# Optimization experiments

Hardware: AMD Instinct MI355X
Metric: run time of the kernel (lower is better)

Reference implementation:

```python
import jax, jax.numpy as jnp
import numpy as np

MAX_ITER = 15
EPSILON = 1e-4


def setup_inputs() -> dict:
    key = jax.random.key(0)
    # [B, N, M] non-negative matching scores
    s = jax.random.uniform(key, (32, 1024, 1024), dtype=jnp.float32)
    return {"s": s}


def reference(s) -> jnp.ndarray:
    # Sinkhorn.forward with defaults -> forward_pai:
    # alternate column-sum (dim=1) and row-sum (dim=2) normalization.
    def body(i, s):
        # i even -> sum over dim 1, i odd -> sum over dim 2
        sum1 = jnp.sum(s, axis=1, keepdims=True)  # [B,1,M]
        sum2 = jnp.sum(s, axis=2, keepdims=True)  # [B,N,1]
        sum_s = jnp.where(i % 2 == 1, sum2, sum1 * jnp.ones_like(sum2))
        # broadcasting: sum1 broadcasts along N, sum2 along M; to keep a
        # single where we expand both to full shape lazily via division.
        denom = jnp.where(i % 2 == 1,
                          jnp.broadcast_to(sum2, s.shape),
                          jnp.broadcast_to(sum1, s.shape))
        return s / (denom + EPSILON)

    # fixed small iteration count; unrolled Python loop keeps each step's
    # reduction axis static (cheaper than the lax.fori where-select above).
    for i in range(MAX_ITER):
        axis = 2 if i % 2 == 1 else 1
        sum_s = jnp.sum(s, axis=axis, keepdims=True)
        s = s / (sum_s + EPSILON)
    return s
```

## Files before the change

kernel.cpp:

```cpp
#include <hip/hip_runtime.h>


#define EPSF 1e-4f
constexpr int B_      = 32;
constexpr int N_      = 1024;
constexpr int M_      = 1024;
constexpr int ICHUNK  = 32;
constexpr int NCHUNKS = N_ / ICHUNK;
constexpr int THREADS = 256;

typedef _Float16 half4v __attribute__((ext_vector_type(4)));
typedef _Float16 half8v __attribute__((ext_vector_type(8)));
typedef float    f32x4  __attribute__((ext_vector_type(4)));

__global__ __launch_bounds__(THREADS)
void colsum_conv_kernel(const float* __restrict__ s0,
                        _Float16* __restrict__ sh,
                        float* __restrict__ upart)
{
    const int bid = blockIdx.x, t = threadIdx.x;
    const int b = bid % B_, chunk = bid / B_;
    const int i0 = chunk * ICHUNK;

    const size_t base4 = ((size_t)b * N_ + i0) * (M_ / 4);
    const f32x4* s4 = reinterpret_cast<const f32x4*>(s0) + base4;
    half4v*      o4 = reinterpret_cast<half4v*>(sh) + base4;

    f32x4 acc = {0.f, 0.f, 0.f, 0.f};
    #pragma unroll 4
    for (int i = 0; i < ICHUNK; ++i) {
        const f32x4 sv = s4[(size_t)i * (M_ / 4) + t];
        acc += sv;
        half4v h;
        h[0] = (_Float16)sv.x; h[1] = (_Float16)sv.y;
        h[2] = (_Float16)sv.z; h[3] = (_Float16)sv.w;
        o4[(size_t)i * (M_ / 4) + t] = h;
    }
    reinterpret_cast<f32x4*>(upart + ((size_t)b * NCHUNKS + chunk) * M_)[t] = acc;
}

__global__ __launch_bounds__(THREADS)
void colsum_f16_kernel(const _Float16* __restrict__ sh,
                       const float* __restrict__ rprev,
                       const float* __restrict__ vacc,
                       float* __restrict__ rout,
                       float* __restrict__ upart,
                       int mode)
{
    __shared__ float rS[ICHUNK];
    const int bid = blockIdx.x, t = threadIdx.x;
    const int b = bid % B_, chunk = bid / B_;
    const int i0 = chunk * ICHUNK;

    if (t < ICHUNK) {
        const int gi = b * N_ + i0 + t;
        const float v  = vacc[gi];
        const float rp = (mode == 1) ? 1.0f : rprev[gi];
        const float r  = rp / (rp * v + EPSF);
        rout[gi] = r;
        rS[t] = r;
    }
    __syncthreads();

    const half4v* srow = reinterpret_cast<const half4v*>(sh)
                       + ((size_t)b * N_ + i0) * (M_ / 4);
    f32x4 acc = {0.f, 0.f, 0.f, 0.f};
    #pragma unroll 8
    for (int i = 0; i < ICHUNK; ++i) {
        const float  r  = rS[i];
        const half4v s4 = srow[(size_t)i * (M_ / 4) + t];
        acc.x += r * (float)s4[0]; acc.y += r * (float)s4[1];
        acc.z += r * (float)s4[2]; acc.w += r * (float)s4[3];
    }
    reinterpret_cast<f32x4*>(upart + ((size_t)b * NCHUNKS + chunk) * M_)[t] = acc;
}

__global__ __launch_bounds__(THREADS)
void rowsum_f16_kernel(const _Float16* __restrict__ sh,
                       const float* __restrict__ cprev,
                       const float* __restrict__ upart,
                       float* __restrict__ cout,
                       float* __restrict__ vacc,
                       int mode)
{
    __shared__ float cS[M_];
    const int bid = blockIdx.x, t = threadIdx.x;
    const int b = bid % B_, chunk = bid / B_;
    const int i0 = chunk * ICHUNK;

    {
        f32x4 u4 = {0.f, 0.f, 0.f, 0.f};
        const f32x4* up = reinterpret_cast<const f32x4*>(upart + (size_t)b * NCHUNKS * M_);
        #pragma unroll 8
        for (int ch = 0; ch < NCHUNKS; ++ch)
            u4 += up[ch * (M_ / 4) + t];

        f32x4 cp4 = {1.f, 1.f, 1.f, 1.f};
        if (mode != 1)
            cp4 = reinterpret_cast<const f32x4*>(cprev + b * M_)[t];
        f32x4 c4;
        c4.x = cp4.x / (cp4.x * u4.x + EPSF);
        c4.y = cp4.y / (cp4.y * u4.y + EPSF);
        c4.z = cp4.z / (cp4.z * u4.z + EPSF);
        c4.w = cp4.w / (cp4.w * u4.w + EPSF);
        reinterpret_cast<f32x4*>(cS)[t] = c4;
        if (chunk == 0)
            reinterpret_cast<f32x4*>(cout + b * M_)[t] = c4;
    }
    __syncthreads();

    const int wave = t >> 6, lane = t & 63;
    constexpr int RPW = ICHUNK / 4;

    const f32x4* cS4 = reinterpret_cast<const f32x4*>(cS);
    f32x4 creg[2][2];
    #pragma unroll
    for (int q = 0; q < 2; ++q) {
        creg[q][0] = cS4[2 * (q * 64 + lane)];
        creg[q][1] = cS4[2 * (q * 64 + lane) + 1];
    }

    const half8v* sbase =
        reinterpret_cast<const half8v*>(sh) + (size_t)b * N_ * (M_ / 8);
    #pragma unroll 2
    for (int rw = 0; rw < RPW; ++rw) {
        const int i = i0 + wave * RPW + rw;
        const half8v* row = sbase + (size_t)i * (M_ / 8);
        float sum = 0.f;
        #pragma unroll
        for (int q = 0; q < 2; ++q) {
            const half8v s8 = row[q * 64 + lane];
            sum += (float)s8[0] * creg[q][0].x + (float)s8[1] * creg[q][0].y
                 + (float)s8[2] * creg[q][0].z + (float)s8[3] * creg[q][0].w
                 + (float)s8[4] * creg[q][1].x + (float)s8[5] * creg[q][1].y
                 + (float)s8[6] * creg[q][1].z + (float)s8[7] * creg[q][1].w;
        }
        #pragma unroll
        for (int off = 32; off > 0; off >>= 1)
            sum += __shfl_down(sum, off, 64);
        if (lane == 0)
            vacc[b * N_ + i] = sum;
    }
}

__global__ __launch_bounds__(THREADS)
void colsum_kernel(const float* __restrict__ s0,
                   const float* __restrict__ rprev,
                   const float* __restrict__ vacc,
                   float* __restrict__ rout,
                   float* __restrict__ upart,
                   int mode)
{
    __shared__ float rS[ICHUNK];
    const int bid = blockIdx.x, t = threadIdx.x;
    const int b = bid % B_, chunk = bid / B_;
    const int i0 = chunk * ICHUNK;

    if (t < ICHUNK) {
        const int gi = b * N_ + i0 + t;
        float r;
        if (mode == 0) r = 1.0f;
        else {
            const float v  = vacc[gi];
            const float rp = (mode == 1) ? 1.0f : rprev[gi];
            r = rp / (rp * v + EPSF);
            rout[gi] = r;
        }
        rS[t] = r;
    }
    __syncthreads();

    const f32x4* srow =
        reinterpret_cast<const f32x4*>(s0) + ((size_t)b * N_ + i0) * (M_ / 4);
    f32x4 acc = {0.f, 0.f, 0.f, 0.f};
    #pragma unroll 8
    for (int i = 0; i < ICHUNK; ++i) {
        const float r  = rS[i];
        const f32x4 sv = srow[(size_t)i * (M_ / 4) + t];
        acc.x += r * sv.x; acc.y += r * sv.y;
        acc.z += r * sv.z; acc.w += r * sv.w;
    }
    reinterpret_cast<f32x4*>(upart + ((size_t)b * NCHUNKS + chunk) * M_)[t] = acc;
}

__global__ __launch_bounds__(THREADS)
void rowsum_kernel(const float* __restrict__ s0,
                   const float* __restrict__ cprev,
                   const float* __restrict__ upart,
                   float* __restrict__ cout,
                   float* __restrict__ vacc,
                   int mode)
{
    __shared__ float cS[M_];
    const int bid = blockIdx.x, t = threadIdx.x;
    const int b = bid % B_, chunk = bid / B_;
    const int i0 = chunk * ICHUNK;

    {
        f32x4 u4 = {0.f, 0.f, 0.f, 0.f};
        const f32x4* up = reinterpret_cast<const f32x4*>(upart + (size_t)b * NCHUNKS * M_);
        #pragma unroll 8
        for (int ch = 0; ch < NCHUNKS; ++ch)
            u4 += up[ch * (M_ / 4) + t];

        f32x4 cp4 = {1.f, 1.f, 1.f, 1.f};
        if (mode != 1)
            cp4 = reinterpret_cast<const f32x4*>(cprev + b * M_)[t];
        f32x4 c4;
        c4.x = cp4.x / (cp4.x * u4.x + EPSF);
        c4.y = cp4.y / (cp4.y * u4.y + EPSF);
        c4.z = cp4.z / (cp4.z * u4.z + EPSF);
        c4.w = cp4.w / (cp4.w * u4.w + EPSF);
        reinterpret_cast<f32x4*>(cS)[t] = c4;
        if (chunk == 0)
            reinterpret_cast<f32x4*>(cout + b * M_)[t] = c4;
    }
    __syncthreads();

    const int wave = t >> 6, lane = t & 63;
    constexpr int RPW = ICHUNK / 4;
    const f32x4* cS4 = reinterpret_cast<const f32x4*>(cS);
    f32x4 creg[4];
    #pragma unroll
    for (int q = 0; q < 4; ++q)
        creg[q] = cS4[q * 64 + lane];

    const f32x4* sbase =
        reinterpret_cast<const f32x4*>(s0) + (size_t)b * N_ * (M_ / 4);
    for (int rw = 0; rw < RPW; ++rw) {
        const int i = i0 + wave * RPW + rw;
        const f32x4* row = sbase + (size_t)i * (M_ / 4);
        float sum = 0.f;
        #pragma unroll
        for (int q = 0; q < 4; ++q) {
            const f32x4 sv = row[q * 64 + lane];
            sum += sv.x * creg[q].x + sv.y * creg[q].y +
                   sv.z * creg[q].z + sv.w * creg[q].w;
        }
        #pragma unroll
        for (int off = 32; off > 0; off >>= 1)
            sum += __shfl_down(sum, off, 64);
        if (lane == 0)
            vacc[b * N_ + i] = sum;
    }
}

__global__ __launch_bounds__(THREADS)
void final_kernel(const float* __restrict__ s0,
                  const float* __restrict__ cprev,
                  const float* __restrict__ upart,
                  const float* __restrict__ rbuf,
                  float* __restrict__ out)
{
    __shared__ float rS[ICHUNK];
    const int bid = blockIdx.x, t = threadIdx.x;
    const int b = bid % B_, chunk = bid / B_;
    const int i0 = chunk * ICHUNK;

    f32x4 u4 = {0.f, 0.f, 0.f, 0.f};
    const f32x4* up = reinterpret_cast<const f32x4*>(upart + (size_t)b * NCHUNKS * M_);
    #pragma unroll 8
    for (int ch = 0; ch < NCHUNKS; ++ch)
        u4 += up[ch * (M_ / 4) + t];

    const f32x4 cp4 = reinterpret_cast<const f32x4*>(cprev + b * M_)[t];
    f32x4 c4;
    c4.x = cp4.x / (cp4.x * u4.x + EPSF);
    c4.y = cp4.y / (cp4.y * u4.y + EPSF);
    c4.z = cp4.z / (cp4.z * u4.z + EPSF);
    c4.w = cp4.w / (cp4.w * u4.w + EPSF);

    if (t < ICHUNK) rS[t] = rbuf[b * N_ + i0 + t];
    __syncthreads();

    const size_t base4 = ((size_t)b * N_ + i0) * (M_ / 4);
    const f32x4* sp = reinterpret_cast<const f32x4*>(s0) + base4;
    f32x4*       op = reinterpret_cast<f32x4*>(out) + base4;
    #pragma unroll 4
    for (int i = 0; i < ICHUNK; ++i) {
        const float r  = rS[i];
        const f32x4 sv = sp[(size_t)i * (M_ / 4) + t];
        f32x4 o;
        o.x = r * sv.x * c4.x;
        o.y = r * sv.y * c4.y;
        o.z = r * sv.z * c4.z;
        o.w = r * sv.w * c4.w;
        __builtin_nontemporal_store(o, op + (size_t)i * (M_ / 4) + t);
    }
}

extern "C" void kernel_launch(void* const* d_in, const int* in_sizes, int n_in,
                              void* d_out, int out_size, void* d_ws, size_t ws_size,
                              hipStream_t stream)
{
    const float* s0  = (const float*)d_in[0];
    float*       out = (float*)d_out;

    constexpr size_t F16_BYTES = (size_t)B_ * N_ * M_ * 2;
    constexpr size_t UPART_FLOATS = (size_t)B_ * NCHUNKS * M_;
    constexpr size_t VEC_BYTES = (UPART_FLOATS + 5 * (size_t)B_ * 1024) * sizeof(float);
    const bool useF16 = ws_size >= F16_BYTES + VEC_BYTES;

    _Float16* sh  = useF16 ? (_Float16*)d_ws : nullptr;
    float*    vec = useF16 ? (float*)((char*)d_ws + F16_BYTES) : (float*)d_ws;

    float* upart = vec;
    float* vacc  = upart + UPART_FLOATS;
    float* rbuf0 = vacc  + B_ * 1024;
    float* rbuf1 = rbuf0 + B_ * 1024;
    float* cbuf0 = rbuf1 + B_ * 1024;
    float* cbuf1 = cbuf0 + B_ * 1024;

    const dim3 grid(B_ * NCHUNKS);
    const dim3 block(THREADS);

    if (useF16)
        colsum_conv_kernel<<<grid, block, 0, stream>>>(s0, sh, upart);
    else
        colsum_kernel<<<grid, block, 0, stream>>>(s0, nullptr, nullptr,
                                                  nullptr, upart, 0);

    if (useF16)
        rowsum_f16_kernel<<<grid, block, 0, stream>>>(sh, nullptr, upart,
                                                      cbuf0, vacc, 1);
    else
        rowsum_kernel<<<grid, block, 0, stream>>>(s0, nullptr, upart,
                                                  cbuf0, vacc, 1);

    if (useF16)
        colsum_f16_kernel<<<grid, block, 0, stream>>>(sh, nullptr, vacc,
                                                      rbuf0, upart, 1);
    else
        colsum_kernel<<<grid, block, 0, stream>>>(s0, nullptr, vacc,
                                                  rbuf0, upart, 1);

    int rIdx = 0, cIdx = 0;
    for (int k = 3; k <= 14; ++k) {
        if (k & 1) {
            float* cp = (cIdx == 0) ? cbuf0 : cbuf1;
            float* cn = (cIdx == 0) ? cbuf1 : cbuf0;
            if (useF16)
                rowsum_f16_kernel<<<grid, block, 0, stream>>>(sh, cp, upart, cn, vacc, 2);
            else
                rowsum_kernel<<<grid, block, 0, stream>>>(s0, cp, upart, cn, vacc, 2);
            cIdx ^= 1;
        } else {
            float* rp = (rIdx == 0) ? rbuf0 : rbuf1;
            float* rn = (rIdx == 0) ? rbuf1 : rbuf0;
            if (useF16)
                colsum_f16_kernel<<<grid, block, 0, stream>>>(sh, rp, vacc, rn, upart, 2);
            else
                colsum_kernel<<<grid, block, 0, stream>>>(s0, rp, vacc, rn, upart, 2);
            rIdx ^= 1;
        }
    }

    final_kernel<<<grid, block, 0, stream>>>(
        s0,
        (cIdx == 0) ? cbuf0 : cbuf1,
        upart,
        (rIdx == 0) ? rbuf0 : rbuf1,
        out);
}
```

Baseline: 466.9 us.

## Fuse all Sinkhorn iterations into one persistent kernel with grid barriers

Replaces the 16 per-iteration kernel launches with a single persistent kernel of 1024 blocks that sync through an atomic grid barrier. Each block handles one 32-row chunk, so the row-scaling factors rS and vS stay in shared memory and are no longer written to global buffers. Column partial sums are double-buffered between barriers. This removes launch gaps and kernel drain/fill between phases, but relies on all 1024 blocks being co-resident (launch bounds of 4 blocks per CU) or the spin barrier deadlocks. It also drops the fp32 fallback path and assumes the workspace is large enough.

```diff
diff --git a/kernel.cpp b/kernel.cpp
--- a/kernel.cpp
+++ b/kernel.cpp
@@ -8,284 +8,168 @@
 constexpr int ICHUNK  = 32;
 constexpr int NCHUNKS = N_ / ICHUNK;
 constexpr int THREADS = 256;
+constexpr int NBLOCKS = B_ * NCHUNKS;
 
 typedef _Float16 half4v __attribute__((ext_vector_type(4)));
 typedef _Float16 half8v __attribute__((ext_vector_type(8)));
 typedef float    f32x4  __attribute__((ext_vector_type(4)));
 
-__global__ __launch_bounds__(THREADS)
-void colsum_conv_kernel(const float* __restrict__ s0,
-                        _Float16* __restrict__ sh,
-                        float* __restrict__ upart)
+__device__ __forceinline__ void gridBarrier(unsigned* bar, unsigned gen)
+{
+    __syncthreads();
+    if (threadIdx.x == 0) {
+        unsigned old = __hip_atomic_fetch_add(&bar[0], 1u, __ATOMIC_ACQ_REL,
+                                              __HIP_MEMORY_SCOPE_AGENT);
+        if (old == (unsigned)(NBLOCKS - 1)) {
+            __hip_atomic_store(&bar[0], 0u, __ATOMIC_RELAXED,
+                               __HIP_MEMORY_SCOPE_AGENT);
+            __hip_atomic_fetch_add(&bar[1], 1u, __ATOMIC_RELEASE,
+                                   __HIP_MEMORY_SCOPE_AGENT);
+        } else {
+            while (__hip_atomic_load(&bar[1], __ATOMIC_ACQUIRE,
+                                     __HIP_MEMORY_SCOPE_AGENT) < gen)
+                __builtin_amdgcn_s_sleep(1);
+        }
+    }
+    __syncthreads();
+}
+
+__global__ __launch_bounds__(THREADS, 4)
+void sinkhorn_persistent(const float* __restrict__ s0,
+                         _Float16* __restrict__ sh,
+                         float* __restrict__ upA,
+                         float* __restrict__ upB,
+                         unsigned* __restrict__ bar,
+                         float* __restrict__ out)
 {
     const int bid = blockIdx.x, t = threadIdx.x;
     const int b = bid % B_, chunk = bid / B_;
     const int i0 = chunk * ICHUNK;
 
+    __shared__ float rS[ICHUNK];
+    __shared__ float vS[ICHUNK];
+    __shared__ float cS[M_];
+
     const size_t base4 = ((size_t)b * N_ + i0) * (M_ / 4);
-    const f32x4* s4 = reinterpret_cast<const f32x4*>(s0) + base4;
-    half4v*      o4 = reinterpret_cast<half4v*>(sh) + base4;
+    const size_t upOff = ((size_t)b * NCHUNKS + chunk) * M_;
 
-    f32x4 acc = {0.f, 0.f, 0.f, 0.f};
-    #pragma unroll 4
-    for (int i = 0; i < ICHUNK; ++i) {
-        const f32x4 sv = s4[(size_t)i * (M_ / 4) + t];
-        acc += sv;
-        half4v h;
-        h[0] = (_Float16)sv.x; h[1] = (_Float16)sv.y;
-        h[2] = (_Float16)sv.z; h[3] = (_Float16)sv.w;
-        o4[(size_t)i * (M_ / 4) + t] = h;
+    {
+        const f32x4* s4 = reinterpret_cast<const f32x4*>(s0) + base4;
+        half4v*      o4 = reinterpret_cast<half4v*>(sh) + base4;
+        f32x4 acc = {0.f, 0.f, 0.f, 0.f};
+        #pragma unroll 4
+        for (int i = 0; i < ICHUNK; ++i) {
+            const f32x4 sv = s4[(size_t)i * (M_ / 4) + t];
+            acc += sv;
+            half4v h;
+            h[0] = (_Float16)sv.x; h[1] = (_Float16)sv.y;
+            h[2] = (_Float16)sv.z; h[3] = (_Float16)sv.w;
+            o4[(size_t)i * (M_ / 4) + t] = h;
+        }
+        reinterpret_cast<f32x4*>(upA + upOff)[t] = acc;
     }
-    reinterpret_cast<f32x4*>(upart + ((size_t)b * NCHUNKS + chunk) * M_)[t] = acc;
-}
+    if (t < ICHUNK) rS[t] = 1.0f;
+    f32x4 cp4 = {1.f, 1.f, 1.f, 1.f};
 
-__global__ __launch_bounds__(THREADS)
-void colsum_f16_kernel(const _Float16* __restrict__ sh,
-                       const float* __restrict__ rprev,
-                       const float* __restrict__ vacc,
-                       float* __restrict__ rout,
-                       float* __restrict__ upart,
-                       int mode)
-{
-    __shared__ float rS[ICHUNK];
-    const int bid = blockIdx.x, t = threadIdx.x;
-    const int b = bid % B_, chunk = bid / B_;
-    const int i0 = chunk * ICHUNK;
+    unsigned gen = 1;
+    gridBarrier(bar, gen++);
 
-    if (t < ICHUNK) {
-        const int gi = b * N_ + i0 + t;
-        const float v  = vacc[gi];
-        const float rp = (mode == 1) ? 1.0f : rprev[gi];
-        const float r  = rp / (rp * v + EPSF);
-        rout[gi] = r;
-        rS[t] = r;
+    const float* upR = upA;
+    float*       upW = upB;
+
+    const half8v* sbase8 =
+        reinterpret_cast<const half8v*>(sh) + (size_t)b * N_ * (M_ / 8);
+    const half4v* sbase4 = reinterpret_cast<const half4v*>(sh) + base4;
+    const int wave = t >> 6, lane = t & 63;
+
+    #pragma unroll 1
+    for (int pair = 0; pair < 7; ++pair) {
+        {
+            f32x4 u4 = {0.f, 0.f, 0.f, 0.f};
+            const f32x4* up =
+                reinterpret_cast<const f32x4*>(upR + (size_t)b * NCHUNKS * M_);
+            #pragma unroll 8
+            for (int ch = 0; ch < NCHUNKS; ++ch)
+                u4 += up[ch * (M_ / 4) + t];
+            f32x4 c4;
+            c4.x = cp4.x / (cp4.x * u4.x + EPSF);
+            c4.y = cp4.y / (cp4.y * u4.y + EPSF);
+            c4.z = cp4.z / (cp4.z * u4.z + EPSF);
+            c4.w = cp4.w / (cp4.w * u4.w + EPSF);
+            cp4 = c4;
+            reinterpret_cast<f32x4*>(cS)[t] = c4;
+        }
+        __syncthreads();
+        {
+            const f32x4* cS4 = reinterpret_cast<const f32x4*>(cS);
+            f32x4 creg[2][2];
+            #pragma unroll
+            for (int q = 0; q < 2; ++q) {
+                creg[q][0] = cS4[2 * (q * 64 + lane)];
+                creg[q][1] = cS4[2 * (q * 64 + lane) + 1];
+            }
+            #pragma unroll 2
+            for (int rw = 0; rw < ICHUNK / 4; ++rw) {
+                const int il = wave * (ICHUNK / 4) + rw;
+                const half8v* row = sbase8 + (size_t)(i0 + il) * (M_ / 8);
+                float sum = 0.f;
+                #pragma unroll
+                for (int q = 0; q < 2; ++q) {
+                    const half8v s8 = row[q * 64 + lane];
+                    sum += (float)s8[0] * creg[q][0].x + (float)s8[1] * creg[q][0].y
+                         + (float)s8[2] * creg[q][0].z + (float)s8[3] * creg[q][0].w
+                         + (float)s8[4] * creg[q][1].x + (float)s8[5] * creg[q][1].y
+                         + (float)s8[6] * creg[q][1].z + (float)s8[7] * creg[q][1].w;
+                }
+                #pragma unroll
+                for (int off = 32; off > 0; off >>= 1)
+                    sum += __shfl_down(sum, off, 64);
+                if (lane == 0) vS[il] = sum;
+            }
+        }
+        __syncthreads();
+        if (t < ICHUNK) rS[t] = rS[t] / (rS[t] * vS[t] + EPSF);
+        __syncthreads();
+        {
+            f32x4 acc = {0.f, 0.f, 0.f, 0.f};
+            #pragma unroll 8
+            for (int i = 0; i < ICHUNK; ++i) {
+                const float  r  = rS[i];
+                const half4v s4 = sbase4[(size_t)i * (M_ / 4) + t];
+                acc.x += r * (float)s4[0]; acc.y += r * (float)s4[1];
+                acc.z += r * (float)s4[2]; acc.w += r * (float)s4[3];
+            }
+            reinterpret_cast<f32x4*>(upW + upOff)[t] = acc;
+        }
+        gridBarrier(bar, gen++);
+        float* tmp = const_cast<float*>(upR); upR = upW; upW = tmp;
     }
-    __syncthreads();
-
-    const half4v* srow = reinterpret_cast<const half4v*>(sh)
-                       + ((size_t)b * N_ + i0) * (M_ / 4);
-    f32x4 acc = {0.f, 0.f, 0.f, 0.f};
-    #pragma unroll 8
-    for (int i = 0; i < ICHUNK; ++i) {
-        const float  r  = rS[i];
-        const half4v s4 = srow[(size_t)i * (M_ / 4) + t];
-        acc.x += r * (float)s4[0]; acc.y += r * (float)s4[1];
-        acc.z += r * (float)s4[2]; acc.w += r * (float)s4[3];
-    }
-    reinterpret_cast<f32x4*>(upart + ((size_t)b * NCHUNKS + chunk) * M_)[t] = acc;
-}
-
-__global__ __launch_bounds__(THREADS)
-void rowsum_f16_kernel(const _Float16* __restrict__ sh,
-                       const float* __restrict__ cprev,
-                       const float* __restrict__ upart,
-                       float* __restrict__ cout,
-                       float* __restrict__ vacc,
-                       int mode)
-{
-    __shared__ float cS[M_];
-    const int bid = blockIdx.x, t = threadIdx.x;
-    const int b = bid % B_, chunk = bid / B_;
-    const int i0 = chunk * ICHUNK;
 
     {
         f32x4 u4 = {0.f, 0.f, 0.f, 0.f};
-        const f32x4* up = reinterpret_cast<const f32x4*>(upart + (size_t)b * NCHUNKS * M_);
+        const f32x4* up =
+            reinterpret_cast<const f32x4*>(upR + (size_t)b * NCHUNKS * M_);
         #pragma unroll 8
         for (int ch = 0; ch < NCHUNKS; ++ch)
             u4 += up[ch * (M_ / 4) + t];
-
-        f32x4 cp4 = {1.f, 1.f, 1.f, 1.f};
-        if (mode != 1)
-            cp4 = reinterpret_cast<const f32x4*>(cprev + b * M_)[t];
         f32x4 c4;
         c4.x = cp4.x / (cp4.x * u4.x + EPSF);
         c4.y = cp4.y / (cp4.y * u4.y + EPSF);
         c4.z = cp4.z / (cp4.z * u4.z + EPSF);
         c4.w = cp4.w / (cp4.w * u4.w + EPSF);
-        reinterpret_cast<f32x4*>(cS)[t] = c4;
-        if (chunk == 0)
-            reinterpret_cast<f32x4*>(cout + b * M_)[t] = c4;
-    }
-    __syncthreads();
 
-    const int wave = t >> 6, lane = t & 63;
-    constexpr int RPW = ICHUNK / 4;
-
-    const f32x4* cS4 = reinterpret_cast<const f32x4*>(cS);
-    f32x4 creg[2][2];
-    #pragma unroll
-    for (int q = 0; q < 2; ++q) {
-        creg[q][0] = cS4[2 * (q * 64 + lane)];
-        creg[q][1] = cS4[2 * (q * 64 + lane) + 1];
-    }
-
-    const half8v* sbase =
-        reinterpret_cast<const half8v*>(sh) + (size_t)b * N_ * (M_ / 8);
-    #pragma unroll 2
-    for (int rw = 0; rw < RPW; ++rw) {
-        const int i = i0 + wave * RPW + rw;
-        const half8v* row = sbase + (size_t)i * (M_ / 8);
-        float sum = 0.f;
-        #pragma unroll
-        for (int q = 0; q < 2; ++q) {
-            const half8v s8 = row[q * 64 + lane];
-            sum += (float)s8[0] * creg[q][0].x + (float)s8[1] * creg[q][0].y
-                 + (float)s8[2] * creg[q][0].z + (float)s8[3] * creg[q][0].w
-                 + (float)s8[4] * creg[q][1].x + (float)s8[5] * creg[q][1].y
-                 + (float)s8[6] * creg[q][1].z + (float)s8[7] * creg[q][1].w;
+        f32x4* op = reinterpret_cast<f32x4*>(out) + base4;
+        #pragma unroll 4
+        for (int i = 0; i < ICHUNK; ++i) {
+            const float  r  = rS[i];
+            const half4v s4 = sbase4[(size_t)i * (M_ / 4) + t];
+            f32x4 o;
+            o.x = r * (float)s4[0] * c4.x;
+            o.y = r * (float)s4[1] * c4.y;
+            o.z = r * (float)s4[2] * c4.z;
+            o.w = r * (float)s4[3] * c4.w;
+            __builtin_nontemporal_store(o, op + (size_t)i * (M_ / 4) + t);
         }
-        #pragma unroll
-        for (int off = 32; off > 0; off >>= 1)
-            sum += __shfl_down(sum, off, 64);
-        if (lane == 0)
-            vacc[b * N_ + i] = sum;
-    }
-}
-
-__global__ __launch_bounds__(THREADS)
-void colsum_kernel(const float* __restrict__ s0,
-                   const float* __restrict__ rprev,
-                   const float* __restrict__ vacc,
-                   float* __restrict__ rout,
-                   float* __restrict__ upart,
-                   int mode)
-{
-    __shared__ float rS[ICHUNK];
-    const int bid = blockIdx.x, t = threadIdx.x;
-    const int b = bid % B_, chunk = bid / B_;
-    const int i0 = chunk * ICHUNK;
-
-    if (t < ICHUNK) {
-        const int gi = b * N_ + i0 + t;
-        float r;
-        if (mode == 0) r = 1.0f;
-        else {
-            const float v  = vacc[gi];
-            const float rp = (mode == 1) ? 1.0f : rprev[gi];
-            r = rp / (rp * v + EPSF);
-            rout[gi] = r;
-        }
-        rS[t] = r;
-    }
-    __syncthreads();
-
-    const f32x4* srow =
-        reinterpret_cast<const f32x4*>(s0) + ((size_t)b * N_ + i0) * (M_ / 4);
-    f32x4 acc = {0.f, 0.f, 0.f, 0.f};
-    #pragma unroll 8
-    for (int i = 0; i < ICHUNK; ++i) {
-        const float r  = rS[i];
-        const f32x4 sv = srow[(size_t)i * (M_ / 4) + t];
-        acc.x += r * sv.x; acc.y += r * sv.y;
-        acc.z += r * sv.z; acc.w += r * sv.w;
-    }
-    reinterpret_cast<f32x4*>(upart + ((size_t)b * NCHUNKS + chunk) * M_)[t] = acc;
-}
-
-__global__ __launch_bounds__(THREADS)
-void rowsum_kernel(const float* __restrict__ s0,
-                   const float* __restrict__ cprev,
-                   const float* __restrict__ upart,
-                   float* __restrict__ cout,
-                   float* __restrict__ vacc,
-                   int mode)
-{
-    __shared__ float cS[M_];
-    const int bid = blockIdx.x, t = threadIdx.x;
-    const int b = bid % B_, chunk = bid / B_;
-    const int i0 = chunk * ICHUNK;
-
-    {
-        f32x4 u4 = {0.f, 0.f, 0.f, 0.f};
-        const f32x4* up = reinterpret_cast<const f32x4*>(upart + (size_t)b * NCHUNKS * M_);
-        #pragma unroll 8
-        for (int ch = 0; ch < NCHUNKS; ++ch)
-            u4 += up[ch * (M_ / 4) + t];
-
-        f32x4 cp4 = {1.f, 1.f, 1.f, 1.f};
-        if (mode != 1)
-            cp4 = reinterpret_cast<const f32x4*>(cprev + b * M_)[t];
-        f32x4 c4;
-        c4.x = cp4.x / (cp4.x * u4.x + EPSF);
-        c4.y = cp4.y / (cp4.y * u4.y + EPSF);
-        c4.z = cp4.z / (cp4.z * u4.z + EPSF);
-        c4.w = cp4.w / (cp4.w * u4.w + EPSF);
-        reinterpret_cast<f32x4*>(cS)[t] = c4;
-        if (chunk == 0)
-            reinterpret_cast<f32x4*>(cout + b * M_)[t] = c4;
-    }
-    __syncthreads();
-
-    const int wave = t >> 6, lane = t & 63;
-    constexpr int RPW = ICHUNK / 4;
-    const f32x4* cS4 = reinterpret_cast<const f32x4*>(cS);
-    f32x4 creg[4];
-    #pragma unroll
-    for (int q = 0; q < 4; ++q)
-        creg[q] = cS4[q * 64 + lane];
-
-    const f32x4* sbase =
-        reinterpret_cast<const f32x4*>(s0) + (size_t)b * N_ * (M_ / 4);
-    for (int rw = 0; rw < RPW; ++rw) {
-        const int i = i0 + wave * RPW + rw;
-        const f32x4* row = sbase + (size_t)i * (M_ / 4);
-        float sum = 0.f;
-        #pragma unroll
-        for (int q = 0; q < 4; ++q) {
-            const f32x4 sv = row[q * 64 + lane];
-            sum += sv.x * creg[q].x + sv.y * creg[q].y +
-                   sv.z * creg[q].z + sv.w * creg[q].w;
-        }
-        #pragma unroll
-        for (int off = 32; off > 0; off >>= 1)
-            sum += __shfl_down(sum, off, 64);
-        if (lane == 0)
-            vacc[b * N_ + i] = sum;
-    }
-}
-
-__global__ __launch_bounds__(THREADS)
-void final_kernel(const float* __restrict__ s0,
-                  const float* __restrict__ cprev,
-                  const float* __restrict__ upart,
-                  const float* __restrict__ rbuf,
-                  float* __restrict__ out)
-{
-    __shared__ float rS[ICHUNK];
-    const int bid = blockIdx.x, t = threadIdx.x;
-    const int b = bid % B_, chunk = bid / B_;
-    const int i0 = chunk * ICHUNK;
-
-    f32x4 u4 = {0.f, 0.f, 0.f, 0.f};
-    const f32x4* up = reinterpret_cast<const f32x4*>(upart + (size_t)b * NCHUNKS * M_);
-    #pragma unroll 8
-    for (int ch = 0; ch < NCHUNKS; ++ch)
-        u4 += up[ch * (M_ / 4) + t];
-
-    const f32x4 cp4 = reinterpret_cast<const f32x4*>(cprev + b * M_)[t];
-    f32x4 c4;
-    c4.x = cp4.x / (cp4.x * u4.x + EPSF);
-    c4.y = cp4.y / (cp4.y * u4.y + EPSF);
-    c4.z = cp4.z / (cp4.z * u4.z + EPSF);
-    c4.w = cp4.w / (cp4.w * u4.w + EPSF);
-
-    if (t < ICHUNK) rS[t] = rbuf[b * N_ + i0 + t];
-    __syncthreads();
-
-    const size_t base4 = ((size_t)b * N_ + i0) * (M_ / 4);
-    const f32x4* sp = reinterpret_cast<const f32x4*>(s0) + base4;
-    f32x4*       op = reinterpret_cast<f32x4*>(out) + base4;
-    #pragma unroll 4
-    for (int i = 0; i < ICHUNK; ++i) {
-        const float r  = rS[i];
-        const f32x4 sv = sp[(size_t)i * (M_ / 4) + t];
-        f32x4 o;
-        o.x = r * sv.x * c4.x;
-        o.y = r * sv.y * c4.y;
-        o.z = r * sv.z * c4.z;
-        o.w = r * sv.w * c4.w;
-        __builtin_nontemporal_store(o, op + (size_t)i * (M_ / 4) + t);
     }
 }
 
@@ -297,68 +181,14 @@
     float*       out = (float*)d_out;
 
     constexpr size_t F16_BYTES = (size_t)B_ * N_ * M_ * 2;
-    constexpr size_t UPART_FLOATS = (size_t)B_ * NCHUNKS * M_;
-    constexpr size_t VEC_BYTES = (UPART_FLOATS + 5 * (size_t)B_ * 1024) * sizeof(float);
-    const bool useF16 = ws_size >= F16_BYTES + VEC_BYTES;
+    constexpr size_t UP_FLOATS = (size_t)B_ * NCHUNKS * M_;
+    _Float16* sh  = (_Float16*)d_ws;
+    float*    upA = (float*)((char*)d_ws + F16_BYTES);
+    float*    upB = upA + UP_FLOATS;
+    unsigned* bar = (unsigned*)(upB + UP_FLOATS);
 
-    _Float16* sh  = useF16 ? (_Float16*)d_ws : nullptr;
-    float*    vec = useF16 ? (float*)((char*)d_ws + F16_BYTES) : (float*)d_ws;
+    hipMemsetAsync(bar, 0, 2 * sizeof(unsigned), stream);
 
-    float* upart = vec;
-    float* vacc  = upart + UPART_FLOATS;
-    float* rbuf0 = vacc  + B_ * 1024;
-    float* rbuf1 = rbuf0 + B_ * 1024;
-    float* cbuf0 = rbuf1 + B_ * 1024;
-    float* cbuf1 = cbuf0 + B_ * 1024;
-
-    const dim3 grid(B_ * NCHUNKS);
-    const dim3 block(THREADS);
-
-    if (useF16)
-        colsum_conv_kernel<<<grid, block, 0, stream>>>(s0, sh, upart);
-    else
-        colsum_kernel<<<grid, block, 0, stream>>>(s0, nullptr, nullptr,
-                                                  nullptr, upart, 0);
-
-    if (useF16)
-        rowsum_f16_kernel<<<grid, block, 0, stream>>>(sh, nullptr, upart,
-                                                      cbuf0, vacc, 1);
-    else
-        rowsum_kernel<<<grid, block, 0, stream>>>(s0, nullptr, upart,
-                                                  cbuf0, vacc, 1);
-
-    if (useF16)
-        colsum_f16_kernel<<<grid, block, 0, stream>>>(sh, nullptr, vacc,
-                                                      rbuf0, upart, 1);
-    else
-        colsum_kernel<<<grid, block, 0, stream>>>(s0, nullptr, vacc,
-                                                  rbuf0, upart, 1);
-
-    int rIdx = 0, cIdx = 0;
-    for (int k = 3; k <= 14; ++k) {
-        if (k & 1) {
-            float* cp = (cIdx == 0) ? cbuf0 : cbuf1;
-            float* cn = (cIdx == 0) ? cbuf1 : cbuf0;
-            if (useF16)
-                rowsum_f16_kernel<<<grid, block, 0, stream>>>(sh, cp, upart, cn, vacc, 2);
-            else
-                rowsum_kernel<<<grid, block, 0, stream>>>(s0, cp, upart, cn, vacc, 2);
-            cIdx ^= 1;
-        } else {
-            float* rp = (rIdx == 0) ? rbuf0 : rbuf1;
-            float* rn = (rIdx == 0) ? rbuf1 : rbuf0;
-            if (useF16)
-                colsum_f16_kernel<<<grid, block, 0, stream>>>(sh, rp, vacc, rn, upart, 2);
-            else
-                colsum_kernel<<<grid, block, 0, stream>>>(s0, rp, vacc, rn, upart, 2);
-            rIdx ^= 1;
-        }
-    }
-
-    final_kernel<<<grid, block, 0, stream>>>(
-        s0,
-        (cIdx == 0) ? cbuf0 : cbuf1,
-        upart,
-        (rIdx == 0) ? rbuf0 : rbuf1,
-        out);
+    sinkhorn_persistent<<<dim3(NBLOCKS), dim3(THREADS), 0, stream>>>(
+        s0, sh, upA, upB, bar, out);
 }
```

Result: slower. 1.581 ms (+238.7%).
